# Kernel tuning notes

Hardware: AMD Instinct MI355X
Metric: run time of the kernel (lower is better)

## Reference

```python
import jax, jax.numpy as jnp
import numpy as np

N_NODES = 10000
N_EDGES = 160000
HIDDEN = 512
N_LAYERS = 5


def setup_inputs() -> dict:
    key = jax.random.key(0)
    ks = jax.random.split(key, 12)
    return {
        "feat": jax.random.normal(ks[0], (N_NODES, HIDDEN), dtype=jnp.float32),
        "adj_row": jax.random.randint(ks[1], (N_EDGES,), 0, N_NODES, dtype=jnp.int32),
        "adj_col": jax.random.randint(ks[2], (N_EDGES,), 0, N_NODES, dtype=jnp.int32),
        "adj_val": jax.random.uniform(ks[3], (N_EDGES,), dtype=jnp.float32),
        "Wg": jax.random.normal(ks[4], (N_LAYERS, HIDDEN, HIDDEN), dtype=jnp.float32) * 0.02,
        "bg": jnp.zeros((N_LAYERS, HIDDEN), dtype=jnp.float32),
        "vw1": jax.random.normal(ks[5], (HIDDEN, HIDDEN), dtype=jnp.float32) * 0.02,
        "vb1": jnp.zeros((HIDDEN,), dtype=jnp.float32),
        "vw2": jax.random.normal(ks[6], (HIDDEN, 1), dtype=jnp.float32) * 0.02,
        "vb2": jnp.zeros((1,), dtype=jnp.float32),
    }


def _spmm(adj_row, adj_col, adj_val, x, n):
    # out[r] = sum_e adj_val[e] * x[adj_col[e]] for edges with adj_row[e] == r
    gathered = adj_val[:, None] * x[adj_col]  # [E, H]
    return jax.ops.segment_sum(gathered, adj_row, num_segments=n)


def reference(feat, adj_row, adj_col, adj_val, Wg, bg, vw1, vb1, vw2, vb2):
    n = feat.shape[0]
    x = feat
    for i in range(N_LAYERS):  # 5 structurally identical GraphConv layers
        h = x @ Wg[i]                                 # dense GEMM [N,H]
        agg = _spmm(adj_row, adj_col, adj_val, h, n)  # sparse aggregation
        x = jax.nn.relu(agg + bg[i])                  # bias + ReLU (dropout = eval identity)
    h = jax.nn.relu(x @ vw1 + vb1)
    return jax.nn.sigmoid(h @ vw2 + vb2)  # [N, 1]
```

## Files before the change

### kernel.cpp

```cpp
#include <hip/hip_runtime.h>

#define H 512
#define NNODES 10000
#define NEDGES 160000
#define NLAYERS 5
#define CAP 64

typedef __attribute__((ext_vector_type(8))) short short8;
typedef __attribute__((ext_vector_type(4))) float floatx4;

__device__ inline unsigned short f2bf(float v) {
    union { float f; unsigned int u; } x; x.f = v;
    unsigned int r = (x.u + 0x7fffu + ((x.u >> 16) & 1u)) >> 16;
    return (unsigned short)r;
}
__device__ inline float bf2f(unsigned short u) {
    union { unsigned int u; float f; } x; x.u = ((unsigned int)u) << 16; return x.f;
}
__device__ inline void gl_lds16(const void* g, void* l) {
    __builtin_amdgcn_global_load_lds((const __attribute__((address_space(1))) void*)g,
                                     (__attribute__((address_space(3))) void*)l, 16, 0, 0);
}

#define ZB 5040
#define CB 5000
#define TB 1536
#define OB 40

__global__ __launch_bounds__(256)
void prep_fused(int* __restrict__ zero_base, const float* __restrict__ feat,
                unsigned short* __restrict__ x, const float* __restrict__ Wg,
                const float* __restrict__ vw1, unsigned short* __restrict__ Wt,
                float* __restrict__ outz) {
    __shared__ float tile[32][33];
    const int b = blockIdx.x;
    const int t = threadIdx.x;
    if (b < ZB) {
        int i = b * 256 + t;
        if (i < 1290000) zero_base[i] = 0;
    } else if (b < ZB + CB) {
        int i = (b - ZB) * 256 + t;
        float4 v = ((const float4*)feat)[i];
        ushort4 o;
        o.x = f2bf(v.x); o.y = f2bf(v.y); o.z = f2bf(v.z); o.w = f2bf(v.w);
        ((ushort4*)x)[i] = o;
    } else if (b < ZB + CB + TB) {
        const int bb = b - ZB - CB;
        const int z = bb >> 8;
        const int rem = bb & 255;
        const int by = (rem >> 4) * 32;
        const int bx = (rem & 15) * 32;
        const float* in = (z < NLAYERS) ? (Wg + (size_t)z * H * H) : vw1;
        unsigned short* out = Wt + (size_t)z * H * H;
        const int tx = t & 31, ty = t >> 5;
        for (int i = ty; i < 32; i += 8)
            tile[i][tx] = in[(size_t)(by + i) * H + bx + tx];
        __syncthreads();
        for (int i = ty; i < 32; i += 8)
            out[(size_t)(bx + i) * H + by + tx] = f2bf(tile[tx][i]);
    } else {
        int i = (b - ZB - CB - TB) * 256 + t;
        if (i < NNODES) outz[i] = 0.f;
    }
}

__global__ void edge_scatter_direct(const int* __restrict__ rows, const int* __restrict__ colsin,
                                    const float* __restrict__ valsin, int* __restrict__ fill,
                                    int* __restrict__ colsout, float* __restrict__ valsout, int n) {
    int i = blockIdx.x * blockDim.x + threadIdx.x;
    if (i < n) {
        int r = rows[i];
        int pos = atomicAdd(&fill[r], 1);
        if (pos < CAP) {
            colsout[r * CAP + pos] = colsin[i];
            valsout[r * CAP + pos] = valsin[i];
        }
    }
}

__global__ __launch_bounds__(256)
void gemm_bf16_xcd(const unsigned short* __restrict__ A, const unsigned short* __restrict__ Bt,
                   unsigned short* __restrict__ C, const float* __restrict__ bias,
                   const float* __restrict__ w2, float* __restrict__ outp,
                   int mode, int M) {
    __shared__ __align__(16) unsigned short lsA[64 * 64];
    __shared__ __align__(16) unsigned short lsB[64 * 64];
    const int L = blockIdx.x;
    const int m_low = L & 7;
    const int rest = L >> 3;
    const int n = rest & 7;
    const int m_high = rest >> 3;
    const int m = m_high * 8 + m_low;
    const int tileM = m * 64, tileN = n * 64;

    const int t = threadIdx.x;
    const int lane = t & 63;
    const int wave = t >> 6;
    const int wm = wave >> 1, wn = wave & 1;
    const int quad = lane >> 4, r16 = lane & 15;

    floatx4 acc[2][2] = {};

    const unsigned short* ap[2];
#pragma unroll
    for (int q = 0; q < 2; ++q) {
        const int c = t + 256 * q;
        const int row = c >> 3;
        int g = tileM + row; if (g >= M) g = M - 1;
        ap[q] = A + (size_t)g * 512 + (((c & 7) ^ (row & 7)) * 8);
    }
    const unsigned short* bp[2];
#pragma unroll
    for (int q = 0; q < 2; ++q) {
        const int c = t + 256 * q;
        const int row = c >> 3;
        bp[q] = Bt + (size_t)(tileN + row) * 512 + (((c & 7) ^ (row & 7)) * 8);
    }

    for (int k0 = 0; k0 < 512; k0 += 64) {
        gl_lds16(ap[0] + k0, lsA + (size_t)t * 8);
        gl_lds16(ap[1] + k0, lsA + (size_t)(t + 256) * 8);
        gl_lds16(bp[0] + k0, lsB + (size_t)t * 8);
        gl_lds16(bp[1] + k0, lsB + (size_t)(t + 256) * 8);
        __syncthreads();

        short8 af[2][2], bfr[2][2];
#pragma unroll
        for (int i = 0; i < 2; ++i) {
            const int row = wm * 32 + i * 16 + r16;
#pragma unroll
            for (int kk = 0; kk < 2; ++kk) {
                const int kcw = kk * 4 + quad;
                af[i][kk] = *(const short8*)&lsA[(size_t)(row * 8 + (kcw ^ (row & 7))) * 8];
            }
        }
#pragma unroll
        for (int j = 0; j < 2; ++j) {
            const int row = wn * 32 + j * 16 + r16;
#pragma unroll
            for (int kk = 0; kk < 2; ++kk) {
                const int kcw = kk * 4 + quad;
                bfr[j][kk] = *(const short8*)&lsB[(size_t)(row * 8 + (kcw ^ (row & 7))) * 8];
            }
        }
#pragma unroll
        for (int kk = 0; kk < 2; ++kk)
#pragma unroll
            for (int i = 0; i < 2; ++i)
#pragma unroll
                for (int j = 0; j < 2; ++j)
                    acc[i][j] = __builtin_amdgcn_mfma_f32_16x16x32_bf16(af[i][kk], bfr[j][kk], acc[i][j], 0, 0, 0);
        __syncthreads();
    }

    if (mode == 2) {
        float part[2][4] = {};
#pragma unroll
        for (int i = 0; i < 2; ++i) {
#pragma unroll
            for (int j = 0; j < 2; ++j) {
                const int col = tileN + wn * 32 + j * 16 + r16;
                const float bcol = bias[col];
                const float wcol = w2[col];
#pragma unroll
                for (int reg = 0; reg < 4; ++reg) {
                    float v = fmaxf(acc[i][j][reg] + bcol, 0.f);
                    part[i][reg] += v * wcol;
                }
            }
        }
#pragma unroll
        for (int off = 1; off <= 8; off <<= 1)
#pragma unroll
            for (int i = 0; i < 2; ++i)
#pragma unroll
                for (int reg = 0; reg < 4; ++reg)
                    part[i][reg] += __shfl_xor(part[i][reg], off, 64);
        if (r16 == 0) {
#pragma unroll
            for (int i = 0; i < 2; ++i)
#pragma unroll
                for (int reg = 0; reg < 4; ++reg) {
                    const int row = tileM + wm * 32 + i * 16 + quad * 4 + reg;
                    if (row < M) atomicAdd(&outp[row], part[i][reg]);
                }
        }
    } else {
#pragma unroll
        for (int i = 0; i < 2; ++i) {
#pragma unroll
            for (int j = 0; j < 2; ++j) {
                const int col = tileN + wn * 32 + j * 16 + r16;
#pragma unroll
                for (int reg = 0; reg < 4; ++reg) {
                    const int row = tileM + wm * 32 + i * 16 + quad * 4 + reg;
                    if (row < M) C[(size_t)row * 512 + col] = f2bf(acc[i][j][reg]);
                }
            }
        }
    }
}

__global__ __launch_bounds__(256)
void spmm_pad(const int* __restrict__ fill, const int* __restrict__ cols,
              const float* __restrict__ vals, const unsigned short* __restrict__ hmat,
              const float* __restrict__ bias, unsigned short* __restrict__ xout) {
    const int wave = threadIdx.x >> 6, lane = threadIdx.x & 63;
    const int r = blockIdx.x * 4 + wave;
    if (r >= NNODES) return;
    int cnt = fill[r];
    cnt = __builtin_amdgcn_readfirstlane(cnt);
    const int s = r * CAP;
    const int e = s + ((cnt + 3) & ~3);
    const int cb = lane * 8;
    float acc[8] = {0.f, 0.f, 0.f, 0.f, 0.f, 0.f, 0.f, 0.f};

    for (int i = s; i < e; i += 4) {
        int c[4]; float v[4]; short8 g[4];
#pragma unroll
        for (int u = 0; u < 4; ++u) { c[u] = cols[i + u]; v[u] = vals[i + u]; }
#pragma unroll
        for (int u = 0; u < 4; ++u) g[u] = *(const short8*)(hmat + (size_t)c[u] * H + cb);
#pragma unroll
        for (int u = 0; u < 4; ++u)
#pragma unroll
            for (int j = 0; j < 8; ++j) acc[j] += v[u] * bf2f((unsigned short)g[u][j]);
    }

    short8 o;
#pragma unroll
    for (int j = 0; j < 8; ++j)
        o[j] = (short)f2bf(fmaxf(acc[j] + bias[cb + j], 0.f));
    *(short8*)(xout + (size_t)r * H + cb) = o;
}

__global__ __launch_bounds__(256)
void sigmoid_tail(float* __restrict__ out, const float* __restrict__ b2, int n) {
    int i = blockIdx.x * blockDim.x + threadIdx.x;
    if (i < n) out[i] = 1.f / (1.f + expf(-(out[i] + b2[0])));
}

extern "C" void kernel_launch(void* const* d_in, const int* in_sizes, int n_in,
                              void* d_out, int out_size, void* d_ws, size_t ws_size,
                              hipStream_t stream) {
    (void)in_sizes; (void)n_in; (void)out_size; (void)ws_size;
    const float* feat   = (const float*)d_in[0];
    const int* adj_row  = (const int*)d_in[1];
    const int* adj_col  = (const int*)d_in[2];
    const float* adj_val= (const float*)d_in[3];
    const float* Wg     = (const float*)d_in[4];
    const float* bg     = (const float*)d_in[5];
    const float* vw1    = (const float*)d_in[6];
    const float* vb1    = (const float*)d_in[7];
    const float* vw2    = (const float*)d_in[8];
    const float* vb2    = (const float*)d_in[9];
    float* out = (float*)d_out;

    char* ws = (char*)d_ws;
    unsigned short* x  = (unsigned short*)(ws + 0);
    unsigned short* h  = (unsigned short*)(ws + 10240000);
    unsigned short* Wt = (unsigned short*)(ws + 20480000);
    int*   fill    = (int*)(ws + 23625728);
    int*   colsP   = (int*)(ws + 23665728);
    float* valsP   = (float*)(ws + 26225728);

    prep_fused<<<ZB + CB + TB + OB, 256, 0, stream>>>(fill, feat, x, Wg, vw1, Wt, out);
    edge_scatter_direct<<<(NEDGES + 255) / 256, 256, 0, stream>>>(adj_row, adj_col, adj_val,
                                                                  fill, colsP, valsP, NEDGES);

    for (int l = 0; l < NLAYERS; ++l) {
        gemm_bf16_xcd<<<1280, 256, 0, stream>>>(x, Wt + (size_t)l * H * H, h,
                                                nullptr, nullptr, nullptr, 0, NNODES);
        spmm_pad<<<(NNODES + 3) / 4, 256, 0, stream>>>(fill, colsP, valsP, h, bg + (size_t)l * H, x);
    }
    gemm_bf16_xcd<<<1280, 256, 0, stream>>>(x, Wt + (size_t)NLAYERS * H * H, nullptr,
                                            vb1, vw2, out, 2, NNODES);
    sigmoid_tail<<<(NNODES + 255) / 256, 256, 0, stream>>>(out, vb2, NNODES);
}
```

Before: 288.7 us.

## Fuse sigmoid tail into final GEMM via last-block counter; software-pipeline SpMM gathers

Removes the separate sigmoid launch by having the last block of the final GEMM, detected through an atomic counter, apply bias and sigmoid over all outputs. The counter is zeroed by extending the prep kernel's zeroing range by one word. The SpMM inner loop is restructured into a two-stage ping-pong so the next pair of row gathers is issued before the current pair is accumulated, to hide gather latency. The fused tail runs serially in a single block over all 10000 rows and adds fences and a global atomic to every block.

```diff
diff --git a/kernel.cpp b/kernel.cpp
--- a/kernel.cpp
+++ b/kernel.cpp
@@ -37,7 +37,7 @@
     const int t = threadIdx.x;
     if (b < ZB) {
         int i = b * 256 + t;
-        if (i < 1290000) zero_base[i] = 0;
+        if (i < 1290001) zero_base[i] = 0;
     } else if (b < ZB + CB) {
         int i = (b - ZB) * 256 + t;
         float4 v = ((const float4*)feat)[i];
@@ -82,6 +82,7 @@
 void gemm_bf16_xcd(const unsigned short* __restrict__ A, const unsigned short* __restrict__ Bt,
                    unsigned short* __restrict__ C, const float* __restrict__ bias,
                    const float* __restrict__ w2, float* __restrict__ outp,
+                   const float* __restrict__ b2, int* __restrict__ counter,
                    int mode, int M) {
     __shared__ __align__(16) unsigned short lsA[64 * 64];
     __shared__ __align__(16) unsigned short lsB[64 * 64];
@@ -184,6 +185,17 @@
                     const int row = tileM + wm * 32 + i * 16 + quad * 4 + reg;
                     if (row < M) atomicAdd(&outp[row], part[i][reg]);
                 }
+        }
+        __shared__ int lastblk;
+        __threadfence();
+        __syncthreads();
+        if (t == 0) lastblk = (atomicAdd(counter, 1) == gridDim.x - 1);
+        __syncthreads();
+        if (lastblk) {
+            __threadfence();
+            const float bb2 = b2[0];
+            for (int i = t; i < M; i += 256)
+                outp[i] = 1.f / (1.f + expf(-(outp[i] + bb2)));
         }
     } else {
 #pragma unroll
@@ -215,16 +227,35 @@
     const int cb = lane * 8;
     float acc[8] = {0.f, 0.f, 0.f, 0.f, 0.f, 0.f, 0.f, 0.f};
 
+    float vA[2]; short8 gA[2];
+    if (s < e) {
+        int c0 = cols[s], c1 = cols[s + 1];
+        vA[0] = vals[s]; vA[1] = vals[s + 1];
+        gA[0] = *(const short8*)(hmat + (size_t)c0 * H + cb);
+        gA[1] = *(const short8*)(hmat + (size_t)c1 * H + cb);
+    }
     for (int i = s; i < e; i += 4) {
-        int c[4]; float v[4]; short8 g[4];
-#pragma unroll
-        for (int u = 0; u < 4; ++u) { c[u] = cols[i + u]; v[u] = vals[i + u]; }
-#pragma unroll
-        for (int u = 0; u < 4; ++u) g[u] = *(const short8*)(hmat + (size_t)c[u] * H + cb);
-#pragma unroll
-        for (int u = 0; u < 4; ++u)
-#pragma unroll
-            for (int j = 0; j < 8; ++j) acc[j] += v[u] * bf2f((unsigned short)g[u][j]);
+        float vB[2]; short8 gB[2];
+        {
+            int c0 = cols[i + 2], c1 = cols[i + 3];
+            vB[0] = vals[i + 2]; vB[1] = vals[i + 3];
+            gB[0] = *(const short8*)(hmat + (size_t)c0 * H + cb);
+            gB[1] = *(const short8*)(hmat + (size_t)c1 * H + cb);
+        }
+#pragma unroll
+        for (int u = 0; u < 2; ++u)
+#pragma unroll
+            for (int j = 0; j < 8; ++j) acc[j] += vA[u] * bf2f((unsigned short)gA[u][j]);
+        if (i + 4 < e) {
+            int c0 = cols[i + 4], c1 = cols[i + 5];
+            vA[0] = vals[i + 4]; vA[1] = vals[i + 5];
+            gA[0] = *(const short8*)(hmat + (size_t)c0 * H + cb);
+            gA[1] = *(const short8*)(hmat + (size_t)c1 * H + cb);
+        }
+#pragma unroll
+        for (int u = 0; u < 2; ++u)
+#pragma unroll
+            for (int j = 0; j < 8; ++j) acc[j] += vB[u] * bf2f((unsigned short)gB[u][j]);
     }
 
     short8 o;
@@ -232,12 +263,6 @@
     for (int j = 0; j < 8; ++j)
         o[j] = (short)f2bf(fmaxf(acc[j] + bias[cb + j], 0.f));
     *(short8*)(xout + (size_t)r * H + cb) = o;
-}
-
-__global__ __launch_bounds__(256)
-void sigmoid_tail(float* __restrict__ out, const float* __restrict__ b2, int n) {
-    int i = blockIdx.x * blockDim.x + threadIdx.x;
-    if (i < n) out[i] = 1.f / (1.f + expf(-(out[i] + b2[0])));
 }
 
 extern "C" void kernel_launch(void* const* d_in, const int* in_sizes, int n_in,
@@ -263,6 +288,7 @@
     int*   fill    = (int*)(ws + 23625728);
     int*   colsP   = (int*)(ws + 23665728);
     float* valsP   = (float*)(ws + 26225728);
+    int*   counter = (int*)(ws + 28785728);
 
     prep_fused<<<ZB + CB + TB + OB, 256, 0, stream>>>(fill, feat, x, Wg, vw1, Wt, out);
     edge_scatter_direct<<<(NEDGES + 255) / 256, 256, 0, stream>>>(adj_row, adj_col, adj_val,
@@ -270,10 +296,10 @@
 
     for (int l = 0; l < NLAYERS; ++l) {
         gemm_bf16_xcd<<<1280, 256, 0, stream>>>(x, Wt + (size_t)l * H * H, h,
-                                                nullptr, nullptr, nullptr, 0, NNODES);
+                                                nullptr, nullptr, nullptr, nullptr, nullptr,
+                                                0, NNODES);
         spmm_pad<<<(NNODES + 3) / 4, 256, 0, stream>>>(fill, colsP, valsP, h, bg + (size_t)l * H, x);
     }
     gemm_bf16_xcd<<<1280, 256, 0, stream>>>(x, Wt + (size_t)NLAYERS * H * H, nullptr,
-                                            vb1, vw2, out, 2, NNODES);
-    sigmoid_tail<<<(NNODES + 255) / 256, 256, 0, stream>>>(out, vb2, NNODES);
-}
+                                            vb1, vw2, out, vb2, counter, 2, NNODES);
+}
```

After: 374.9 us. 1.3x slower.
